# Kernel tuning notes

Measured on AMD Instinct MI355X. Metric: run time of the kernel, lower is better.

## Reference

```python
import jax, jax.numpy as jnp
import numpy as np

B, T, D, E = 4, 8192, 2048, 64


def setup_inputs() -> dict:
    key = jax.random.key(0)
    k1, k2 = jax.random.split(key)
    x = jax.random.normal(k1, (B, T, D), dtype=jnp.float32)
    kernel_DE = jax.random.normal(k2, (D, E), dtype=jnp.float32) * 0.02
    return {"x": x, "kernel_DE": kernel_DE, "num_experts_per_tok": 8}


def reference(x, kernel_DE, num_experts_per_tok):
    dtype = x.dtype
    # router logits: (B,T,E)
    router_logits_BTE = jnp.einsum("BTD,DE->BTE", x, kernel_DE)
    # gating probs in fp32 for numerical stability
    activated_gating_BTE = jax.nn.softmax(router_logits_BTE.astype(jnp.float32), axis=-1)
    # top-k experts per token
    weights_BTX, selected_experts_BTX = jax.lax.top_k(activated_gating_BTE, num_experts_per_tok)
    # renormalize selected weights via softmax in model dtype (faithful to source)
    normalized_weights_BTX = jax.nn.softmax(weights_BTX.astype(dtype), axis=-1)
    return (normalized_weights_BTX, selected_experts_BTX)
```

## Files before the change

### kernel.cpp

```cpp
#include <hip/hip_runtime.h>
#include <math.h>

#define NTOK  32768
#define DDIM  2048
#define NEXP  64
#define TOPK  8
#define GAP_THR  1e-4f
#define LIST_CAP 16384

#define WFRAG_OFF  1024
#define WFRAG_SZ   (64 * 4 * 2048)
#define LIST_OFF   (WFRAG_OFF + WFRAG_SZ)

typedef __attribute__((ext_vector_type(8))) short s8_t;
typedef __attribute__((ext_vector_type(4))) float f4_t;

__device__ __forceinline__ unsigned short f2bf(float f) {
  const unsigned u = __builtin_bit_cast(unsigned, f);
  const unsigned r = u + 0x7FFFu + ((u >> 16) & 1u);
  return (unsigned short)(r >> 16);
}

__global__ void wprep(const float* __restrict__ w, unsigned short* __restrict__ wf,
                      int* __restrict__ cnt) {
  if (blockIdx.x == 0 && threadIdx.x == 0) cnt[0] = 0;
  const int ks   = blockIdx.x;
  const int eg   = threadIdx.x >> 6;
  const int lane = threadIdx.x & 63;
  const int kb   = ks * 32 + ((lane >> 4) << 3);
  const int e    = (eg << 4) + (lane & 15);
  s8_t h, l;
#pragma unroll
  for (int j = 0; j < 8; ++j) {
    const float v = w[(size_t)(kb + j) * NEXP + e];
    const unsigned short hb = f2bf(v);
    const float hf = __builtin_bit_cast(float, (unsigned)hb << 16);
    h[j] = (short)hb;
    l[j] = (short)f2bf(v - hf);
  }
  unsigned short* base = wf + (size_t)(ks * 4 + eg) * 1024 + lane * 8;
  *(s8_t*)(base)       = h;
  *(s8_t*)(base + 512) = l;
}

__global__ __launch_bounds__(256, 2) void router_main(
    const float* __restrict__ x, const unsigned short* __restrict__ wf,
    float* __restrict__ out, int* __restrict__ cnt, int* __restrict__ list) {
  __shared__ float llds[64 * 68];

  const int tid  = threadIdx.x;
  const int lane = tid & 63;
  const int wave = tid >> 6;
  const int col  = lane & 15;
  const int kgrp = lane >> 4;
  const int wtok = blockIdx.x * 64 + wave * 16;

  f4_t acc[4];
#pragma unroll
  for (int eg = 0; eg < 4; ++eg) acc[eg] = (f4_t){0.f, 0.f, 0.f, 0.f};

  const float* xp = x + (size_t)(wtok + col) * DDIM + (kgrp << 3);

#pragma unroll 2
  for (int ks = 0; ks < DDIM / 32; ++ks) {
    const float4 v0 = *(const float4*)(xp + ks * 32);
    const float4 v1 = *(const float4*)(xp + ks * 32 + 4);
    s8_t ah, al;
    {
      const float xv[8] = {v0.x, v0.y, v0.z, v0.w, v1.x, v1.y, v1.z, v1.w};
#pragma unroll
      for (int j = 0; j < 8; ++j) {
        const unsigned short hb = f2bf(xv[j]);
        const float hf = __builtin_bit_cast(float, (unsigned)hb << 16);
        ah[j] = (short)hb;
        al[j] = (short)f2bf(xv[j] - hf);
      }
    }
    const unsigned short* wb = wf + (size_t)ks * 4096 + lane * 8;
#pragma unroll
    for (int eg = 0; eg < 4; ++eg) {
      const s8_t bh = *(const s8_t*)(wb + eg * 1024);
      const s8_t bl = *(const s8_t*)(wb + eg * 1024 + 512);
      acc[eg] = __builtin_amdgcn_mfma_f32_16x16x32_bf16(ah, bh, acc[eg], 0, 0, 0);
      acc[eg] = __builtin_amdgcn_mfma_f32_16x16x32_bf16(al, bh, acc[eg], 0, 0, 0);
      acc[eg] = __builtin_amdgcn_mfma_f32_16x16x32_bf16(ah, bl, acc[eg], 0, 0, 0);
    }
  }

#pragma unroll
  for (int eg = 0; eg < 4; ++eg)
#pragma unroll
    for (int r = 0; r < 4; ++r)
      llds[(wave * 16 + kgrp * 4 + r) * 68 + eg * 16 + col] = acc[eg][r];
  __syncthreads();

  float* out_w = out;
  float* out_i = out + (size_t)NTOK * TOPK;

#pragma unroll 1
  for (int t = 0; t < 16; ++t) {
    const int tok = wtok + t;
    const float v = llds[(wave * 16 + t) * 68 + lane];

    float m = v;
#pragma unroll
    for (int off = 32; off; off >>= 1) m = fmaxf(m, __shfl_xor(m, off));
    const float ex = __expf(v - m);
    float s = ex;
#pragma unroll
    for (int off = 32; off; off >>= 1) s += __shfl_xor(s, off);
    float pw = ex / s;
    float lw = v;
    int   ii = lane;

    float selp[TOPK + 1];
    float sell[TOPK + 1];
    int   seli[TOPK + 1];
#pragma unroll
    for (int r = 0; r < TOPK + 1; ++r) {
      float bp = pw; float bl = lw; int bi = ii;
#pragma unroll
      for (int off = 32; off; off >>= 1) {
        const float op = __shfl_xor(bp, off);
        const float ol = __shfl_xor(bl, off);
        const int   oi = __shfl_xor(bi, off);
        const bool take = (op > bp) || (op == bp && oi < bi);
        bp = take ? op : bp;
        bl = take ? ol : bl;
        bi = take ? oi : bi;
      }
      selp[r] = bp; sell[r] = bl; seli[r] = bi;
      if (lane == bi) pw = -__builtin_inff();
    }

    bool contested = false;
#pragma unroll
    for (int k = 0; k < TOPK; ++k)
      contested |= (sell[k] - sell[k + 1]) <= GAP_THR;

    const float mm = selp[0];
    float ssum = 0.0f;
#pragma unroll
    for (int k = 0; k < TOPK; ++k) ssum += __expf(selp[k] - mm);
    float myv = selp[0];
    int   myi = seli[0];
#pragma unroll
    for (int k = 1; k < TOPK; ++k)
      if (lane == k) { myv = selp[k]; myi = seli[k]; }
    if (lane < TOPK) {
      out_w[(size_t)tok * TOPK + lane] = __expf(myv - mm) / ssum;
      out_i[(size_t)tok * TOPK + lane] = (float)myi;
    }

    if (contested && lane == 0) {
      const int idx = atomicAdd(cnt, 1);
      if (idx < LIST_CAP) list[idx] = tok;
    }
  }
}

__global__ __launch_bounds__(256, 1) void router_fix(
    const float* __restrict__ x, const float* __restrict__ w,
    float* __restrict__ out, const int* __restrict__ cnt,
    const int* __restrict__ list) {
  const int lane = threadIdx.x & 63;
  const int wave = threadIdx.x >> 6;
  const int gw   = blockIdx.x * 4 + wave;
  const int NW   = gridDim.x * 4;

  int n = cnt[0];
  if (n > LIST_CAP) n = LIST_CAP;

  float* out_w = out;
  float* out_i = out + (size_t)NTOK * TOPK;

  for (int i = gw; i < n; i += NW) {
    const int tok = list[i];
    const float* xr = x + (size_t)tok * DDIM;
    double a0 = 0.0, a1 = 0.0, a2 = 0.0, a3 = 0.0;
#pragma unroll 4
    for (int d4 = 0; d4 < DDIM / 4; ++d4) {
      const float4 xv = *(const float4*)(xr + d4 * 4);
      const int r = d4 * 4;
      a0 = fma((double)xv.x, (double)w[(r + 0) * NEXP + lane], a0);
      a1 = fma((double)xv.y, (double)w[(r + 1) * NEXP + lane], a1);
      a2 = fma((double)xv.z, (double)w[(r + 2) * NEXP + lane], a2);
      a3 = fma((double)xv.w, (double)w[(r + 3) * NEXP + lane], a3);
    }
    const double a = (a0 + a1) + (a2 + a3);

    double dm = a;
#pragma unroll
    for (int off = 32; off; off >>= 1) dm = fmax(dm, __shfl_xor(dm, off));
    const double dex = exp(a - dm);
    double ds = dex;
#pragma unroll
    for (int off = 32; off; off >>= 1) ds += __shfl_xor(ds, off);
    double dpv = dex / ds;

    double dselv[TOPK];
    int    dseli[TOPK];
#pragma unroll
    for (int r = 0; r < TOPK; ++r) {
      double bv = dpv;
      int    bi = lane;
#pragma unroll
      for (int off = 32; off; off >>= 1) {
        const double ov = __shfl_xor(bv, off);
        const int    oi = __shfl_xor(bi, off);
        const bool take = (ov > bv) || (ov == bv && oi < bi);
        bv = take ? ov : bv;
        bi = take ? oi : bi;
      }
      dselv[r] = bv;
      dseli[r] = bi;
      if (lane == bi) dpv = -1.0e300;
    }
    const double dmm = dselv[0];
    double dssum = 0.0;
#pragma unroll
    for (int k = 0; k < TOPK; ++k) dssum += exp(dselv[k] - dmm);
    double myv = dselv[0];
    int    myi = dseli[0];
#pragma unroll
    for (int k = 1; k < TOPK; ++k)
      if (lane == k) { myv = dselv[k]; myi = dseli[k]; }
    if (lane < TOPK) {
      out_w[(size_t)tok * TOPK + lane] = (float)(exp(myv - dmm) / dssum);
      out_i[(size_t)tok * TOPK + lane] = (float)myi;
    }
  }
}

extern "C" void kernel_launch(void* const* d_in, const int* in_sizes, int n_in,
                              void* d_out, int out_size, void* d_ws, size_t ws_size,
                              hipStream_t stream) {
  const float* x = (const float*)d_in[0];
  const float* w = (const float*)d_in[1];
  int* cnt = (int*)d_ws;
  unsigned short* wfrag = (unsigned short*)((char*)d_ws + WFRAG_OFF);
  int* list = (int*)((char*)d_ws + LIST_OFF);

  wprep<<<dim3(64), dim3(256), 0, stream>>>(w, wfrag, cnt);
  router_main<<<dim3(NTOK / 64), dim3(256), 0, stream>>>(
      x, wfrag, (float*)d_out, cnt, list);
  router_fix<<<dim3(256), dim3(256), 0, stream>>>(
      x, w, (float*)d_out, cnt, list);
}
```

Baseline: 565.4 us.

## Double-buffer x and weight tiles in LDS via async global_load_lds

The main router GEMM loop now streams x and the pre-split bf16 weight fragments into double-buffered LDS with direct global-to-LDS loads. The next chunk is prefetched while MFMAs run on the current one. The four waves share the weight tile instead of each fetching it separately, and the bf16 hi/lo split is done with packed bit ops, with the low part truncated rather than rounded. The aim is to hide global-memory latency and cut redundant weight traffic. In exchange it adds a barrier per chunk and raises LDS use to about 64KB per block. The truncated low word slightly changes the logits, a risk for tokens near the gap threshold.

```diff
diff --git a/kernel.cpp b/kernel.cpp
--- a/kernel.cpp
+++ b/kernel.cpp
@@ -12,13 +12,39 @@
 #define WFRAG_SZ   (64 * 4 * 2048)
 #define LIST_OFF   (WFRAG_OFF + WFRAG_SZ)
 
+#define CK      2
+#define NCHUNK  (DDIM / 32 / CK)
+
 typedef __attribute__((ext_vector_type(8))) short s8_t;
 typedef __attribute__((ext_vector_type(4))) float f4_t;
+typedef __attribute__((ext_vector_type(4))) unsigned int u4_t;
+
+typedef const __attribute__((address_space(1))) unsigned int* as1p;
+typedef __attribute__((address_space(3))) unsigned int* as3p;
+
+__device__ __forceinline__ void gl2lds16(const void* g, void* l) {
+  __builtin_amdgcn_global_load_lds((as1p)g, (as3p)l, 16, 0, 0);
+}
 
 __device__ __forceinline__ unsigned short f2bf(float f) {
   const unsigned u = __builtin_bit_cast(unsigned, f);
   const unsigned r = u + 0x7FFFu + ((u >> 16) & 1u);
   return (unsigned short)(r >> 16);
+}
+
+struct bfpair { unsigned hi, lo; };
+__device__ __forceinline__ bfpair split2(float a, float b) {
+  const unsigned ua = __builtin_bit_cast(unsigned, a);
+  const unsigned ub = __builtin_bit_cast(unsigned, b);
+  const unsigned ra = ua + 0x7FFFu + ((ua >> 16) & 1u);
+  const unsigned rb = ub + 0x7FFFu + ((ub >> 16) & 1u);
+  bfpair r;
+  r.hi = (ra >> 16) | (rb & 0xFFFF0000u);
+  const float fa = a - __builtin_bit_cast(float, ra & 0xFFFF0000u);
+  const float fb = b - __builtin_bit_cast(float, rb & 0xFFFF0000u);
+  r.lo = (__builtin_bit_cast(unsigned, fa) >> 16) |
+         (__builtin_bit_cast(unsigned, fb) & 0xFFFF0000u);
+  return r;
 }
 
 __global__ void wprep(const float* __restrict__ w, unsigned short* __restrict__ wf,
@@ -44,9 +70,15 @@
 }
 
 __global__ __launch_bounds__(256, 2) void router_main(
-    const float* __restrict__ x, const unsigned short* __restrict__ wf,
+    const float* __restrict__ x, const unsigned short* __restrict__ wfg,
     float* __restrict__ out, int* __restrict__ cnt, int* __restrict__ list) {
-  __shared__ float llds[64 * 68];
+  __shared__ union {
+    struct {
+      float xb[2][4][CK * 512];
+      unsigned short wb[2][CK * 4096];
+    } s;
+    float ll[64 * 68];
+  } u;
 
   const int tid  = threadIdx.x;
   const int lane = tid & 63;
@@ -59,39 +91,74 @@
 #pragma unroll
   for (int eg = 0; eg < 4; ++eg) acc[eg] = (f4_t){0.f, 0.f, 0.f, 0.f};
 
-  const float* xp = x + (size_t)(wtok + col) * DDIM + (kgrp << 3);
-
-#pragma unroll 2
-  for (int ks = 0; ks < DDIM / 32; ++ks) {
-    const float4 v0 = *(const float4*)(xp + ks * 32);
-    const float4 v1 = *(const float4*)(xp + ks * 32 + 4);
-    s8_t ah, al;
-    {
-      const float xv[8] = {v0.x, v0.y, v0.z, v0.w, v1.x, v1.y, v1.z, v1.w};
-#pragma unroll
-      for (int j = 0; j < 8; ++j) {
-        const unsigned short hb = f2bf(xv[j]);
-        const float hf = __builtin_bit_cast(float, (unsigned)hb << 16);
-        ah[j] = (short)hb;
-        al[j] = (short)f2bf(xv[j] - hf);
+  const float* gx0 = x + (size_t)(wtok + col) * DDIM + (kgrp << 3);
+
+  {
+    float* lx = &u.s.xb[0][wave][0];
+#pragma unroll
+    for (int kk = 0; kk < CK; ++kk) {
+      gl2lds16(gx0 + kk * 32,     lx + kk * 512);
+      gl2lds16(gx0 + kk * 32 + 4, lx + kk * 512 + 256);
+    }
+    const unsigned short* gw = wfg + wave * 2048 + lane * 8;
+    unsigned short* lw = &u.s.wb[0][wave * 2048];
+#pragma unroll
+    for (int j = 0; j < 4; ++j)
+      gl2lds16(gw + j * 512, lw + j * 512);
+  }
+  __syncthreads();
+
+#pragma unroll 1
+  for (int c = 0; c < NCHUNK; ++c) {
+    const int b = c & 1;
+    if (c + 1 < NCHUNK) {
+      const int nb = b ^ 1;
+      const float* gx = gx0 + (size_t)((c + 1) * CK) * 32;
+      float* lx = &u.s.xb[nb][wave][0];
+#pragma unroll
+      for (int kk = 0; kk < CK; ++kk) {
+        gl2lds16(gx + kk * 32,     lx + kk * 512);
+        gl2lds16(gx + kk * 32 + 4, lx + kk * 512 + 256);
       }
-    }
-    const unsigned short* wb = wf + (size_t)ks * 4096 + lane * 8;
-#pragma unroll
-    for (int eg = 0; eg < 4; ++eg) {
-      const s8_t bh = *(const s8_t*)(wb + eg * 1024);
-      const s8_t bl = *(const s8_t*)(wb + eg * 1024 + 512);
-      acc[eg] = __builtin_amdgcn_mfma_f32_16x16x32_bf16(ah, bh, acc[eg], 0, 0, 0);
-      acc[eg] = __builtin_amdgcn_mfma_f32_16x16x32_bf16(al, bh, acc[eg], 0, 0, 0);
-      acc[eg] = __builtin_amdgcn_mfma_f32_16x16x32_bf16(ah, bl, acc[eg], 0, 0, 0);
-    }
+      const unsigned short* gw =
+          wfg + (size_t)((c + 1) * CK) * 4096 + wave * 2048 + lane * 8;
+      unsigned short* lw = &u.s.wb[nb][wave * 2048];
+#pragma unroll
+      for (int j = 0; j < 4; ++j)
+        gl2lds16(gw + j * 512, lw + j * 512);
+    }
+
+    const float* lx = &u.s.xb[b][wave][0];
+    const unsigned short* lw = &u.s.wb[b][0];
+#pragma unroll
+    for (int kk = 0; kk < CK; ++kk) {
+      const float4 v0 = *(const float4*)(lx + kk * 512 + lane * 4);
+      const float4 v1 = *(const float4*)(lx + kk * 512 + 256 + lane * 4);
+      const bfpair p0 = split2(v0.x, v0.y);
+      const bfpair p1 = split2(v0.z, v0.w);
+      const bfpair p2 = split2(v1.x, v1.y);
+      const bfpair p3 = split2(v1.z, v1.w);
+      const u4_t uh = {p0.hi, p1.hi, p2.hi, p3.hi};
+      const u4_t ul = {p0.lo, p1.lo, p2.lo, p3.lo};
+      const s8_t ah = __builtin_bit_cast(s8_t, uh);
+      const s8_t al = __builtin_bit_cast(s8_t, ul);
+#pragma unroll
+      for (int eg = 0; eg < 4; ++eg) {
+        const s8_t bh = *(const s8_t*)(lw + kk * 4096 + eg * 1024 + lane * 8);
+        const s8_t bl = *(const s8_t*)(lw + kk * 4096 + eg * 1024 + 512 + lane * 8);
+        acc[eg] = __builtin_amdgcn_mfma_f32_16x16x32_bf16(ah, bh, acc[eg], 0, 0, 0);
+        acc[eg] = __builtin_amdgcn_mfma_f32_16x16x32_bf16(al, bh, acc[eg], 0, 0, 0);
+        acc[eg] = __builtin_amdgcn_mfma_f32_16x16x32_bf16(ah, bl, acc[eg], 0, 0, 0);
+      }
+    }
+    __syncthreads();
   }
 
 #pragma unroll
   for (int eg = 0; eg < 4; ++eg)
 #pragma unroll
     for (int r = 0; r < 4; ++r)
-      llds[(wave * 16 + kgrp * 4 + r) * 68 + eg * 16 + col] = acc[eg][r];
+      u.ll[(wave * 16 + kgrp * 4 + r) * 68 + eg * 16 + col] = acc[eg][r];
   __syncthreads();
 
   float* out_w = out;
@@ -100,7 +167,7 @@
 #pragma unroll 1
   for (int t = 0; t < 16; ++t) {
     const int tok = wtok + t;
-    const float v = llds[(wave * 16 + t) * 68 + lane];
+    const float v = u.ll[(wave * 16 + t) * 68 + lane];
 
     float m = v;
 #pragma unroll
```

New measurement: 531.3 us. 6.0% less time.
